# Optimization experiments

Measured on AMD Instinct MI355X. Metric: run time of the kernel, lower is better.

The kernel has to match this reference:

```python
import jax, jax.numpy as jnp
import numpy as np

DIM = 512
N_LAYERS = 2
N_HEADS = 8
HEAD_DIM = DIM // N_HEADS
VOCAB = 50257
MAX_SEQ = 2048
N_LEVELS = 3  # len(chunk_sizes)
HID = 4 * DIM
B, S = 2, 1024
STD = 0.02
EPS = 1e-5


def setup_inputs() -> dict:
    key = jax.random.key(0)
    ks = jax.random.split(key, 12)
    f32 = jnp.float32
    inp = {}
    inp["input_ids"] = jax.random.randint(ks[0], (B, S), 0, VOCAB)
    inp["tok_emb"] = jax.random.normal(ks[1], (VOCAB, DIM), f32) * STD  # tied with head
    inp["pos_emb"] = jax.random.normal(ks[2], (MAX_SEQ, DIM), f32) * STD
    # attention projections, stored [in, out] so y = x @ W (math-equivalent to torch x @ W.T)
    inp["Wq"] = jax.random.normal(ks[3], (N_LAYERS, DIM, DIM), f32) * STD
    inp["Wk"] = jax.random.normal(ks[4], (N_LAYERS, DIM, DIM), f32) * STD
    inp["Wv"] = jax.random.normal(ks[5], (N_LAYERS, DIM, DIM), f32) * STD
    inp["Wo"] = jax.random.normal(ks[6], (N_LAYERS, DIM, DIM), f32) * STD
    # layer norms
    inp["ln1_g"] = jnp.ones((N_LAYERS, DIM), f32)
    inp["ln1_b"] = jnp.zeros((N_LAYERS, DIM), f32)
    inp["ln2_g"] = jnp.ones((N_LAYERS, DIM), f32)
    inp["ln2_b"] = jnp.zeros((N_LAYERS, DIM), f32)
    inp["lnf_g"] = jnp.ones((DIM,), f32)
    inp["lnf_b"] = jnp.zeros((DIM,), f32)
    # continuum memory system: N_LEVELS chained MLPs per layer
    inp["W1"] = jax.random.normal(ks[7], (N_LAYERS, N_LEVELS, DIM, HID), f32) * STD
    inp["b1"] = jnp.zeros((N_LAYERS, N_LEVELS, HID), f32)
    inp["W2"] = jax.random.normal(ks[8], (N_LAYERS, N_LEVELS, HID, DIM), f32) * STD
    inp["b2"] = jnp.zeros((N_LAYERS, N_LEVELS, DIM), f32)
    return inp


def layer_norm(x, g, b):
    mu = jnp.mean(x, axis=-1, keepdims=True)
    var = jnp.var(x, axis=-1, keepdims=True)
    return (x - mu) / jnp.sqrt(var + EPS) * g + b


def linear_attention_with_memory(x, Wq, Wk, Wv, Wo):
    # x: [B, S, D]. Fast-weight recurrence: M_t = M_{t-1} + v_t k_t^T ; y_t = M_t q_t
    Bsz, Slen, D = x.shape
    H, hd = N_HEADS, HEAD_DIM

    def proj(W):  # -> [S, B, H, hd] (time-major for scan)
        return jnp.moveaxis((x @ W).reshape(Bsz, Slen, H, hd), 1, 0)

    q, k, v = proj(Wq), proj(Wk), proj(Wv)
    M0 = jnp.zeros((Bsz, H, hd, hd), x.dtype)

    def step(M, qkv):
        q_t, k_t, v_t = qkv
        M = M + jnp.einsum('bhd,bhk->bhdk', v_t, k_t)
        y_t = jnp.einsum('bhdk,bhk->bhd', M, q_t)
        return M, y_t

    _, ys = jax.lax.scan(step, M0, (q, k, v))  # ys: [S, B, H, hd]
    y = jnp.moveaxis(ys, 0, 1).reshape(Bsz, Slen, D)
    return y @ Wo


def cms(x, W1, b1, W2, b2):
    # chained MLP levels (dropout=0 / eval mode)
    for m in range(W1.shape[0]):
        x = jax.nn.gelu(x @ W1[m] + b1[m]) @ W2[m] + b2[m]
    return x


def reference(input_ids, tok_emb, pos_emb, Wq, Wk, Wv, Wo,
              ln1_g, ln1_b, ln2_g, ln2_b, lnf_g, lnf_b,
              W1, b1, W2, b2):
    Bsz, Slen = input_ids.shape
    x = tok_emb[input_ids] + pos_emb[:Slen][None, :, :]
    for l in range(Wq.shape[0]):
        x = x + linear_attention_with_memory(layer_norm(x, ln1_g[l], ln1_b[l]),
                                             Wq[l], Wk[l], Wv[l], Wo[l])
        x = x + cms(layer_norm(x, ln2_g[l], ln2_b[l]), W1[l], b1[l], W2[l], b2[l])
    x = layer_norm(x, lnf_g, lnf_b)
    logits = x @ tok_emb.T  # tied head
    return logits
```

## Files before the change

kernel.cpp:

```cpp
#include <hip/hip_runtime.h>
#include <hip/hip_bf16.h>
#include <cstdint>

using bf16 = __hip_bfloat16;
typedef __attribute__((ext_vector_type(8))) __bf16 bf16x8;
typedef __attribute__((ext_vector_type(4))) float f32x4;
typedef __attribute__((ext_vector_type(4))) unsigned int u32x4;

#define SEQ    1024
#define BATCH  2
#define ROWS   (BATCH*SEQ)
#define DMODEL 512
#define HIDDEN 2048
#define NHEADS 8
#define HD     64
#define VOCABN 50257
#define CHUNK  32
#define NCHUNK (SEQ/CHUNK)
#define QKVW   1536

__device__ __forceinline__ float gelu_tanh(float x) {
  float u = 0.7978845608028654f * (x + 0.044715f * x * x * x);
  return 0.5f * x * (1.0f + tanhf(u));
}

__global__ __launch_bounds__(512, 2)
void head_gemm8(const bf16* __restrict__ A, const bf16* __restrict__ Bt,
                float* __restrict__ C, int N, int ntn)
{
  constexpr int NT = 16;
  __shared__ __align__(16) bf16 Al[2 * 256 * 32];
  __shared__ __align__(16) bf16 Bl[2 * 256 * 32];
  const int t = threadIdx.x, lane = t & 63;
  const int w = t >> 6, wm = w >> 2, wn = w & 3;
  const int tm = blockIdx.x & 7, tn = blockIdx.x >> 3;
  const int arow0 = tm * 256, brow0 = tn * 256;
  const int rA = lane & 15;
  const int ko0 = lane >> 4;
  const int kph = ((ko0 ^ (rA & 3) ^ ((rA >> 2) & 3)) << 4);

  f32x4 acc[2][2][4][2];
#pragma unroll
  for (int i = 0; i < 2; ++i)
#pragma unroll
    for (int j = 0; j < 2; ++j)
#pragma unroll
      for (int m = 0; m < 4; ++m)
#pragma unroll
        for (int n = 0; n < 2; ++n) acc[i][j][m][n] = (f32x4){0.f, 0.f, 0.f, 0.f};

  auto stageA = [&](int s, int half, bf16* dstbuf) {
    int row = t >> 2, ko = t & 3;
    int kosrc = ko ^ (row & 3) ^ ((row >> 2) & 3);
    const bf16* src = A + (size_t)(arow0 + half * 128 + row) * 512 + s * 32 + kosrc * 8;
    bf16* dst = dstbuf + (half * 128 + row) * 32 + ko * 8;
    __builtin_amdgcn_global_load_lds(
        (const __attribute__((address_space(1))) unsigned int*)src,
        (__attribute__((address_space(3))) unsigned int*)dst, 16, 0, 0);
  };
  auto stageB = [&](int s, int half, bf16* dstbuf) {
    int row = t >> 2, ko = t & 3;
    int kosrc = ko ^ (row & 3) ^ ((row >> 2) & 3);
    int br = brow0 + half * 128 + row; br = br < N ? br : N - 1;
    const bf16* src = Bt + (size_t)br * 512 + s * 32 + kosrc * 8;
    bf16* dst = dstbuf + (half * 128 + row) * 32 + ko * 8;
    __builtin_amdgcn_global_load_lds(
        (const __attribute__((address_space(1))) unsigned int*)src,
        (__attribute__((address_space(3))) unsigned int*)dst, 16, 0, 0);
  };

  bf16* Ac = Al;
  bf16* Bc = Bl;
  bf16* An = Al + 8192;
  bf16* Bn = Bl + 8192;

  stageA(0, 0, Ac); stageB(0, 0, Bc); stageA(0, 1, Ac); stageB(0, 1, Bc);
  stageA(1, 0, An); stageB(1, 0, Bn);
  asm volatile("s_waitcnt vmcnt(2)" ::: "memory");
  asm volatile("s_barrier" ::: "memory");

#define PH(MH, NH, AC, BC, STAGE_STMT, WAIT_STMT) do {                          \
    bf16x8 a_[4], b_[2];                                                        \
    _Pragma("unroll") for (int fm = 0; fm < 4; ++fm) {                          \
      const char* ap = (const char*)(AC) +                                      \
          ((MH) * 128 + wm * 64 + fm * 16 + rA) * 64;                           \
      a_[fm] = __builtin_bit_cast(bf16x8, *(const u32x4*)(ap + kph));           \
    }                                                                           \
    _Pragma("unroll") for (int fn = 0; fn < 2; ++fn) {                          \
      const char* bp = (const char*)(BC) +                                      \
          ((NH) * 128 + wn * 32 + fn * 16 + rA) * 64;                           \
      b_[fn] = __builtin_bit_cast(bf16x8, *(const u32x4*)(bp + kph));           \
    }                                                                           \
    STAGE_STMT;                                                                 \
    asm volatile("s_barrier" ::: "memory");                                     \
    asm volatile("s_waitcnt lgkmcnt(0)" ::: "memory");                          \
    __builtin_amdgcn_sched_barrier(0);                                          \
    __builtin_amdgcn_s_setprio(1);                                              \
    _Pragma("unroll") for (int fm = 0; fm < 4; ++fm)                            \
      _Pragma("unroll") for (int fn = 0; fn < 2; ++fn)                          \
        acc[MH][NH][fm][fn] = __builtin_amdgcn_mfma_f32_16x16x32_bf16(          \
            a_[fm], b_[fn], acc[MH][NH][fm][fn], 0, 0, 0);                      \
    __builtin_amdgcn_s_setprio(0);                                              \
    WAIT_STMT;                                                                  \
    asm volatile("s_barrier" ::: "memory");                                     \
  } while (0)

#pragma unroll
  for (int I = 0; I < NT / 2; ++I) {
    const int u = 2 * I;
    PH(0, 0, Ac, Bc, { stageA(u + 1, 1, An); }, {});
    PH(0, 1, Ac, Bc, { stageB(u + 1, 1, Bn); }, {});
    PH(1, 0, Ac, Bc, { if (u + 2 < NT) stageA(u + 2, 0, Ac); }, {});
    PH(1, 1, Ac, Bc, { if (u + 2 < NT) stageB(u + 2, 0, Bc); },
       { if (u + 2 < NT) asm volatile("s_waitcnt vmcnt(2)" ::: "memory");
         else            asm volatile("s_waitcnt vmcnt(0)" ::: "memory"); });
    PH(0, 0, An, Bn, { if (u + 2 < NT) stageA(u + 2, 1, Ac); }, {});
    PH(0, 1, An, Bn, { if (u + 2 < NT) stageB(u + 2, 1, Bc); }, {});
    PH(1, 0, An, Bn, { if (u + 3 < NT) stageA(u + 3, 0, An); }, {});
    PH(1, 1, An, Bn, { if (u + 3 < NT) stageB(u + 3, 0, Bn); },
       { if (u + 2 < NT) {
           if (u + 3 < NT) asm volatile("s_waitcnt vmcnt(2)" ::: "memory");
           else            asm volatile("s_waitcnt vmcnt(0)" ::: "memory");
         } });
  }
#undef PH

#pragma unroll
  for (int mh = 0; mh < 2; ++mh)
#pragma unroll
    for (int fm = 0; fm < 4; ++fm) {
      int row = arow0 + mh * 128 + wm * 64 + fm * 16 + (lane >> 4) * 4;
#pragma unroll
      for (int nh = 0; nh < 2; ++nh)
#pragma unroll
        for (int fn = 0; fn < 2; ++fn) {
          int col = brow0 + nh * 128 + wn * 32 + fn * 16 + (lane & 15);
          if (col < N) {
#pragma unroll
            for (int r = 0; r < 4; ++r)
              C[(size_t)(row + r) * N + col] = acc[mh][nh][fm][fn][r];
          }
        }
    }
}

template<int EPI>
__global__ __launch_bounds__(256, 4)
void gemm_mid(const bf16* __restrict__ A, const bf16* __restrict__ Bt,
              void* __restrict__ Cout, const float* __restrict__ bias,
              int M, int N, int K, int Ks, int ldc, int ntn)
{
  __shared__ __align__(16) bf16 As[128 * 64];
  __shared__ __align__(16) bf16 Bs[64 * 64];
  const int t = threadIdx.x;
  const int lane = t & 63;
  const int w = t >> 6;
  const int wr = w >> 1, wc = w & 1;
  const int tm = blockIdx.x / ntn, tn = blockIdx.x % ntn;
  const int sk = blockIdx.y;
  const int kbeg = sk * Ks;
  const int rA = lane & 15;
  const int ko0 = lane >> 4;

  f32x4 acc[4][2];
#pragma unroll
  for (int m = 0; m < 4; ++m)
#pragma unroll
    for (int n = 0; n < 2; ++n) acc[m][n] = (f32x4){0.f, 0.f, 0.f, 0.f};

  for (int k0 = kbeg; k0 < kbeg + Ks; k0 += 64) {
#pragma unroll
    for (int rep = 0; rep < 4; ++rep) {
      int c = rep * 256 + t;
      int row = c >> 3, ko = c & 7;
      const bf16* ga = A + (size_t)(tm * 128 + row) * K + k0 + (ko ^ (row & 7)) * 8;
      __builtin_amdgcn_global_load_lds(
          (const __attribute__((address_space(1))) unsigned int*)ga,
          (__attribute__((address_space(3))) unsigned int*)(As + row * 64 + ko * 8),
          16, 0, 0);
    }
#pragma unroll
    for (int rep = 0; rep < 2; ++rep) {
      int c = rep * 256 + t;
      int row = c >> 3, ko = c & 7;
      const bf16* gb = Bt + (size_t)(tn * 64 + row) * K + k0 + (ko ^ (row & 7)) * 8;
      __builtin_amdgcn_global_load_lds(
          (const __attribute__((address_space(1))) unsigned int*)gb,
          (__attribute__((address_space(3))) unsigned int*)(Bs + row * 64 + ko * 8),
          16, 0, 0);
    }
    asm volatile("s_waitcnt vmcnt(0)" ::: "memory");
    __syncthreads();

    {
      bf16x8 af[4], bfv[2];
#pragma unroll
      for (int m = 0; m < 4; ++m) {
        int row = wr * 64 + m * 16 + rA;
        af[m] = __builtin_bit_cast(bf16x8,
            *(const u32x4*)((const char*)As + row * 128 + ((ko0 ^ (row & 7)) << 4)));
      }
#pragma unroll
      for (int n = 0; n < 2; ++n) {
        int row = wc * 32 + n * 16 + rA;
        bfv[n] = __builtin_bit_cast(bf16x8,
            *(const u32x4*)((const char*)Bs + row * 128 + ((ko0 ^ (row & 7)) << 4)));
      }
#pragma unroll
      for (int m = 0; m < 4; ++m)
#pragma unroll
        for (int n = 0; n < 2; ++n)
          acc[m][n] = __builtin_amdgcn_mfma_f32_16x16x32_bf16(af[m], bfv[n], acc[m][n], 0, 0, 0);
    }
    {
      bf16x8 af[4], bfv[2];
#pragma unroll
      for (int m = 0; m < 4; ++m) {
        int row = wr * 64 + m * 16 + rA;
        af[m] = __builtin_bit_cast(bf16x8,
            *(const u32x4*)((const char*)As + row * 128 + (((ko0 ^ (row & 7)) << 4) ^ 64)));
      }
#pragma unroll
      for (int n = 0; n < 2; ++n) {
        int row = wc * 32 + n * 16 + rA;
        bfv[n] = __builtin_bit_cast(bf16x8,
            *(const u32x4*)((const char*)Bs + row * 128 + (((ko0 ^ (row & 7)) << 4) ^ 64)));
      }
#pragma unroll
      for (int m = 0; m < 4; ++m)
#pragma unroll
        for (int n = 0; n < 2; ++n)
          acc[m][n] = __builtin_amdgcn_mfma_f32_16x16x32_bf16(af[m], bfv[n], acc[m][n], 0, 0, 0);
    }
    __syncthreads();
  }

#pragma unroll
  for (int m = 0; m < 4; ++m) {
    const int row = tm * 128 + wr * 64 + m * 16 + (lane >> 4) * 4;
#pragma unroll
    for (int n = 0; n < 2; ++n) {
      const int col = tn * 64 + wc * 32 + n * 16 + rA;
#pragma unroll
      for (int r = 0; r < 4; ++r) {
        float v = acc[m][n][r];
        if (EPI == 0) {
          ((float*)Cout)[(size_t)(row + r) * ldc + col] = v;
        } else if (EPI == 1) {
          ((float*)Cout)[(size_t)sk * M * N + (size_t)(row + r) * N + col] = v;
        } else {
          v += bias[col]; v = gelu_tanh(v);
          ((bf16*)Cout)[(size_t)(row + r) * ldc + col] = __float2bfloat16(v);
        }
      }
    }
  }
}

__global__ __launch_bounds__(256)
void reduce_bias_bf16(const float* __restrict__ part, bf16* __restrict__ out,
                      const float* __restrict__ bias)
{
  int i = blockIdx.x * 256 + threadIdx.x;
  const float4* p4 = (const float4*)part;
  const size_t str = (size_t)ROWS * DMODEL / 4;
  float4 v = p4[i];
  float4 v1 = p4[i + str], v2 = p4[i + 2 * str], v3 = p4[i + 3 * str];
  v.x += v1.x + v2.x + v3.x; v.y += v1.y + v2.y + v3.y;
  v.z += v1.z + v2.z + v3.z; v.w += v1.w + v2.w + v3.w;
  float4 bb = ((const float4*)bias)[i & (DMODEL / 4 - 1)];
  v.x += bb.x; v.y += bb.y; v.z += bb.z; v.w += bb.w;
  union { bf16 h[4]; uint2 u; } cv;
  cv.h[0] = __float2bfloat16(v.x); cv.h[1] = __float2bfloat16(v.y);
  cv.h[2] = __float2bfloat16(v.z); cv.h[3] = __float2bfloat16(v.w);
  ((uint2*)out)[i] = cv.u;
}

template<bool BIAS>
__global__ __launch_bounds__(256)
void reduce_resid_ln(const float* __restrict__ part, float* __restrict__ x,
                     const float* __restrict__ bias, const float* __restrict__ g,
                     const float* __restrict__ b, bf16* __restrict__ xn)
{
  int lane = threadIdx.x & 63;
  int row = blockIdx.x * 4 + (threadIdx.x >> 6);
  const float4* p4 = (const float4*)part;
  const size_t str = (size_t)ROWS * DMODEL / 4;
  size_t base = (size_t)row * (DMODEL / 4) + lane * 2;
  float4 a0 = p4[base], a1 = p4[base + 1];
#pragma unroll
  for (int s = 1; s < 4; ++s) {
    float4 q0 = p4[base + s * str], q1 = p4[base + 1 + s * str];
    a0.x += q0.x; a0.y += q0.y; a0.z += q0.z; a0.w += q0.w;
    a1.x += q1.x; a1.y += q1.y; a1.z += q1.z; a1.w += q1.w;
  }
  if (BIAS) {
    float4 b0 = ((const float4*)bias)[lane * 2];
    float4 b1 = ((const float4*)bias)[lane * 2 + 1];
    a0.x += b0.x; a0.y += b0.y; a0.z += b0.z; a0.w += b0.w;
    a1.x += b1.x; a1.y += b1.y; a1.z += b1.z; a1.w += b1.w;
  }
  float4* xr = (float4*)(x + (size_t)row * DMODEL);
  float4 x0 = xr[lane * 2], x1 = xr[lane * 2 + 1];
  x0.x += a0.x; x0.y += a0.y; x0.z += a0.z; x0.w += a0.w;
  x1.x += a1.x; x1.y += a1.y; x1.z += a1.z; x1.w += a1.w;
  xr[lane * 2] = x0; xr[lane * 2 + 1] = x1;
  float s  = x0.x + x0.y + x0.z + x0.w + x1.x + x1.y + x1.z + x1.w;
  float ss = x0.x*x0.x + x0.y*x0.y + x0.z*x0.z + x0.w*x0.w
           + x1.x*x1.x + x1.y*x1.y + x1.z*x1.z + x1.w*x1.w;
#pragma unroll
  for (int off = 32; off > 0; off >>= 1) { s += __shfl_xor(s, off); ss += __shfl_xor(ss, off); }
  float mu = s * (1.f / DMODEL);
  float inv = rsqrtf(ss * (1.f / DMODEL) - mu * mu + 1e-5f);
  int c0 = lane * 8;
  float vv[8] = {x0.x, x0.y, x0.z, x0.w, x1.x, x1.y, x1.z, x1.w};
#pragma unroll
  for (int j = 0; j < 8; ++j)
    xn[(size_t)row * DMODEL + c0 + j] = __float2bfloat16((vv[j] - mu) * inv * g[c0 + j] + b[c0 + j]);
}

__global__ __launch_bounds__(256)
void embed_ln(const int* __restrict__ ids, const float* __restrict__ te,
              const float* __restrict__ pe, const float* __restrict__ g,
              const float* __restrict__ b, float* __restrict__ x, bf16* __restrict__ xn)
{
  int lane = threadIdx.x & 63;
  int row = blockIdx.x * 4 + (threadIdx.x >> 6);
  int sq = row & (SEQ - 1);
  int id = ids[row];
  const float4* tr = (const float4*)(te + (size_t)id * DMODEL);
  const float4* pr = (const float4*)(pe + (size_t)sq * DMODEL);
  float4 x0 = tr[lane * 2], x1 = tr[lane * 2 + 1];
  float4 p0 = pr[lane * 2], p1 = pr[lane * 2 + 1];
  x0.x += p0.x; x0.y += p0.y; x0.z += p0.z; x0.w += p0.w;
  x1.x += p1.x; x1.y += p1.y; x1.z += p1.z; x1.w += p1.w;
  float4* xr = (float4*)(x + (size_t)row * DMODEL);
  xr[lane * 2] = x0; xr[lane * 2 + 1] = x1;
  float s  = x0.x + x0.y + x0.z + x0.w + x1.x + x1.y + x1.z + x1.w;
  float ss = x0.x*x0.x + x0.y*x0.y + x0.z*x0.z + x0.w*x0.w
           + x1.x*x1.x + x1.y*x1.y + x1.z*x1.z + x1.w*x1.w;
#pragma unroll
  for (int off = 32; off > 0; off >>= 1) { s += __shfl_xor(s, off); ss += __shfl_xor(ss, off); }
  float mu = s * (1.f / DMODEL);
  float inv = rsqrtf(ss * (1.f / DMODEL) - mu * mu + 1e-5f);
  int c0 = lane * 8;
  float vv[8] = {x0.x, x0.y, x0.z, x0.w, x1.x, x1.y, x1.z, x1.w};
#pragma unroll
  for (int j = 0; j < 8; ++j)
    xn[(size_t)row * DMODEL + c0 + j] = __float2bfloat16((vv[j] - mu) * inv * g[c0 + j] + b[c0 + j]);
}

__global__ __launch_bounds__(256)
void transpose_cvt(const float* __restrict__ in, bf16* __restrict__ out, int R, int C)
{
  __shared__ float tile[32][33];
  int mat = blockIdx.z;
  const float* src = in + (size_t)mat * R * C;
  bf16* dst = out + (size_t)mat * R * C;
  int c0 = blockIdx.x * 32, r0 = blockIdx.y * 32;
  int tx = threadIdx.x, ty = threadIdx.y;
#pragma unroll
  for (int i = ty; i < 32; i += 8)
    tile[i][tx] = src[(size_t)(r0 + i) * C + c0 + tx];
  __syncthreads();
#pragma unroll
  for (int i = ty; i < 32; i += 8)
    dst[(size_t)(c0 + i) * R + r0 + tx] = __float2bfloat16(tile[tx][i]);
}

__global__ __launch_bounds__(256)
void transpose_qkv(const float* __restrict__ Wq, const float* __restrict__ Wk,
                   const float* __restrict__ Wv, bf16* __restrict__ out)
{
  __shared__ float tile[32][33];
  int z = blockIdx.z;
  int l = z / 3, p = z % 3;
  const float* src = (p == 0 ? Wq : (p == 1 ? Wk : Wv)) + (size_t)l * DMODEL * DMODEL;
  bf16* dst = out + (size_t)l * QKVW * DMODEL + (size_t)p * DMODEL * DMODEL;
  int c0 = blockIdx.x * 32, r0 = blockIdx.y * 32;
  int tx = threadIdx.x, ty = threadIdx.y;
#pragma unroll
  for (int i = ty; i < 32; i += 8)
    tile[i][tx] = src[(size_t)(r0 + i) * DMODEL + c0 + tx];
  __syncthreads();
#pragma unroll
  for (int i = ty; i < 32; i += 8)
    dst[(size_t)(c0 + i) * DMODEL + r0 + tx] = __float2bfloat16(tile[tx][i]);
}

__global__ void cvt_bf16_k(const float* __restrict__ in, bf16* __restrict__ out, int n4)
{
  int i = blockIdx.x * 256 + threadIdx.x;
  if (i >= n4) return;
  float4 v = ((const float4*)in)[i];
  union { bf16 h[4]; uint2 u; } cv;
  cv.h[0] = __float2bfloat16(v.x); cv.h[1] = __float2bfloat16(v.y);
  cv.h[2] = __float2bfloat16(v.z); cv.h[3] = __float2bfloat16(v.w);
  ((uint2*)out)[i] = cv.u;
}

__global__ __launch_bounds__(256)
void scan_ktv(const float* __restrict__ qkv, float* __restrict__ ktv)
{
  int blk = blockIdx.x;
  int c = blk & (NCHUNK - 1), bh = blk >> 5;
  int b = bh >> 3, h = bh & 7;
  __shared__ float ks[CHUNK][64], vs[CHUNK][64];
  int t = threadIdx.x;
  size_t base = ((size_t)(b * SEQ + c * CHUNK)) * QKVW + h * HD;
#pragma unroll
  for (int i = 0; i < CHUNK * 64 / 256; ++i) {
    int idx = i * 256 + t;
    int s = idx >> 6, e = idx & 63;
    ks[s][e] = qkv[base + 512 + (size_t)s * QKVW + e];
    vs[s][e] = qkv[base + 1024 + (size_t)s * QKVW + e];
  }
  __syncthreads();
  int e = t >> 2, d0 = (t & 3) * 16;
  float acc[16];
#pragma unroll
  for (int j = 0; j < 16; ++j) acc[j] = 0.f;
  for (int s = 0; s < CHUNK; ++s) {
    float kv = ks[s][e];
#pragma unroll
    for (int j = 0; j < 16; ++j) acc[j] += kv * vs[s][d0 + j];
  }
  float* o = ktv + (size_t)blk * 4096 + e * 64 + d0;
#pragma unroll
  for (int j = 0; j < 16; ++j) o[j] = acc[j];
}

__global__ __launch_bounds__(256)
void scan_attn(const float* __restrict__ qkv, const float* __restrict__ ktv,
               bf16* __restrict__ y)
{
  int blk = blockIdx.x;
  int c = blk & (NCHUNK - 1), bh = blk >> 5;
  int b = bh >> 3, h = bh & 7;
  __shared__ float qs[CHUNK][65], ks[CHUNK][65], vs[CHUNK][65];
  __shared__ float Ss[CHUNK][CHUNK + 1];
  __shared__ float Ms[64][65];
  int t = threadIdx.x;
  size_t base = ((size_t)(b * SEQ + c * CHUNK)) * QKVW + h * HD;
#pragma unroll
  for (int i = 0; i < CHUNK * 64 / 256; ++i) {
    int idx = i * 256 + t;
    int s = idx >> 6, e = idx & 63;
    qs[s][e] = qkv[base + (size_t)s * QKVW + e];
    ks[s][e] = qkv[base + 512 + (size_t)s * QKVW + e];
    vs[s][e] = qkv[base + 1024 + (size_t)s * QKVW + e];
  }
  {
    int e = t >> 2, d0 = (t & 3) * 16;
    float mp[16];
#pragma unroll
    for (int j = 0; j < 16; ++j) mp[j] = 0.f;
    for (int cp = 0; cp < c; ++cp) {
      const float* p = ktv + ((size_t)bh * NCHUNK + cp) * 4096 + e * 64 + d0;
#pragma unroll
      for (int j = 0; j < 16; ++j) mp[j] += p[j];
    }
#pragma unroll
    for (int j = 0; j < 16; ++j) Ms[e][d0 + j] = mp[j];
  }
  __syncthreads();
  {
    int si = t >> 3, j0 = (t & 7) * 4;
    float sa[4] = {0.f, 0.f, 0.f, 0.f};
    for (int e = 0; e < 64; ++e) {
      float qv = qs[si][e];
#pragma unroll
      for (int j = 0; j < 4; ++j) sa[j] += qv * ks[j0 + j][e];
    }
#pragma unroll
    for (int j = 0; j < 4; ++j) Ss[si][j0 + j] = (j0 + j <= si) ? sa[j] : 0.f;
  }
  __syncthreads();
  {
    int si = t >> 3, d0 = (t & 7) * 8;
    float ya[8];
#pragma unroll
    for (int j = 0; j < 8; ++j) ya[j] = 0.f;
    for (int sp = 0; sp < CHUNK; ++sp) {
      float sv = Ss[si][sp];
#pragma unroll
      for (int j = 0; j < 8; ++j) ya[j] += sv * vs[sp][d0 + j];
    }
    for (int e = 0; e < 64; ++e) {
      float qv = qs[si][e];
#pragma unroll
      for (int j = 0; j < 8; ++j) ya[j] += qv * Ms[e][d0 + j];
    }
    bf16* o = y + ((size_t)(b * SEQ + c * CHUNK + si)) * DMODEL + h * HD + d0;
#pragma unroll
    for (int j = 0; j < 8; ++j) o[j] = __float2bfloat16(ya[j]);
  }
}

extern "C" void kernel_launch(void* const* d_in, const int* in_sizes, int n_in,
                              void* d_out, int out_size, void* d_ws, size_t ws_size,
                              hipStream_t stream)
{
  const int*   ids  = (const int*)  d_in[0];
  const float* tok  = (const float*)d_in[1];
  const float* pos  = (const float*)d_in[2];
  const float* Wq   = (const float*)d_in[3];
  const float* Wk   = (const float*)d_in[4];
  const float* Wv   = (const float*)d_in[5];
  const float* Wo   = (const float*)d_in[6];
  const float* ln1g = (const float*)d_in[7];
  const float* ln1b = (const float*)d_in[8];
  const float* ln2g = (const float*)d_in[9];
  const float* ln2b = (const float*)d_in[10];
  const float* lnfg = (const float*)d_in[11];
  const float* lnfb = (const float*)d_in[12];
  const float* W1   = (const float*)d_in[13];
  const float* b1   = (const float*)d_in[14];
  const float* W2   = (const float*)d_in[15];
  const float* b2   = (const float*)d_in[16];
  float* out = (float*)d_out;

  char* ws = (char*)d_ws;
  size_t off = 0;
  auto alloc = [&](size_t bytes) { void* p = ws + off; off += (bytes + 255) & ~(size_t)255; return p; };
  bf16* QKVt = (bf16*)alloc((size_t)2 * QKVW * 512 * 2);
  bf16* Wot  = (bf16*)alloc((size_t)2 * 512 * 512 * 2);
  bf16* W1t  = (bf16*)alloc((size_t)6 * 512 * 2048 * 2);
  bf16* W2t  = (bf16*)alloc((size_t)6 * 2048 * 512 * 2);
  bf16* tokb = (bf16*)alloc((size_t)VOCABN * 512 * 2);
  float* x   = (float*)alloc((size_t)ROWS * 512 * 4);
  bf16*  xn  = (bf16*) alloc((size_t)ROWS * 512 * 2);
  bf16*  tbuf= (bf16*) alloc((size_t)ROWS * 512 * 2);
  bf16*  hbuf= (bf16*) alloc((size_t)ROWS * 2048 * 2);
  float* qkvf= (float*)alloc((size_t)ROWS * QKVW * 4);
  bf16*  yb  = (bf16*) alloc((size_t)ROWS * 512 * 2);
  float* ktv = (float*)alloc((size_t)16 * NCHUNK * 4096 * 4);
  float* part= (float*)alloc((size_t)4 * ROWS * 512 * 4);

  dim3 tb(32, 8);
  transpose_qkv<<<dim3(16, 16, 6), tb, 0, stream>>>(Wq, Wk, Wv, QKVt);
  transpose_cvt<<<dim3(16, 16, 2), tb, 0, stream>>>(Wo, Wot, 512, 512);
  transpose_cvt<<<dim3(64, 16, 6), tb, 0, stream>>>(W1, W1t, 512, 2048);
  transpose_cvt<<<dim3(16, 64, 6), tb, 0, stream>>>(W2, W2t, 2048, 512);
  int n4 = VOCABN * 512 / 4;
  cvt_bf16_k<<<(n4 + 255) / 256, 256, 0, stream>>>(tok, tokb, n4);

  embed_ln<<<ROWS / 4, 256, 0, stream>>>(ids, tok, pos, ln1g, ln1b, x, xn);

  for (int l = 0; l < 2; ++l) {
    gemm_mid<0><<<dim3(16 * (QKVW / 64)), 256, 0, stream>>>(
        xn, QKVt + (size_t)l * QKVW * 512, qkvf, nullptr, ROWS, QKVW, 512, 512, QKVW, QKVW / 64);
    scan_ktv<<<16 * NCHUNK, 256, 0, stream>>>(qkvf, ktv);
    scan_attn<<<16 * NCHUNK, 256, 0, stream>>>(qkvf, ktv, yb);
    gemm_mid<1><<<dim3(16 * 8, 4), 256, 0, stream>>>(
        yb, Wot + (size_t)l * 512 * 512, part, nullptr, ROWS, 512, 512, 128, 512, 8);
    reduce_resid_ln<false><<<ROWS / 4, 256, 0, stream>>>(
        part, x, nullptr, ln2g + l * 512, ln2b + l * 512, xn);

    const bf16* cur = xn;
    for (int m = 0; m < 3; ++m) {
      int lm = l * 3 + m;
      gemm_mid<2><<<dim3(16 * (2048 / 64)), 256, 0, stream>>>(
          cur, W1t + (size_t)lm * 2048 * 512, hbuf, b1 + (size_t)lm * 2048,
          ROWS, 2048, 512, 512, 2048, 2048 / 64);
      gemm_mid<1><<<dim3(16 * 8, 4), 256, 0, stream>>>(
          hbuf, W2t + (size_t)lm * 512 * 2048, part, nullptr, ROWS, 512, 2048, 512, 512, 8);
      if (m < 2) {
        reduce_bias_bf16<<<ROWS * 512 / 4 / 256, 256, 0, stream>>>(part, tbuf, b2 + (size_t)lm * 512);
        cur = tbuf;
      } else {
        const float* g = (l == 0) ? (ln1g + 512) : lnfg;
        const float* b = (l == 0) ? (ln1b + 512) : lnfb;
        reduce_resid_ln<true><<<ROWS / 4, 256, 0, stream>>>(part, x, b2 + (size_t)lm * 512, g, b, xn);
      }
    }
  }

  int ntn_h = (VOCABN + 255) / 256;
  head_gemm8<<<dim3(8 * ntn_h), 512, 0, stream>>>(xn, tokb, out, VOCABN, ntn_h);
}
```

Before: 653.3 us.

## Replace pipelined 256x256 head GEMM with single-buffered 128x256 tile kernel

Result: faster. 603.8 us (-7.6%).

```diff
diff --git a/kernel.cpp b/kernel.cpp
--- a/kernel.cpp
+++ b/kernel.cpp
@@ -25,123 +25,105 @@
 }
 
 __global__ __launch_bounds__(512, 2)
-void head_gemm8(const bf16* __restrict__ A, const bf16* __restrict__ Bt,
-                float* __restrict__ C, int N, int ntn)
-{
-  constexpr int NT = 16;
-  __shared__ __align__(16) bf16 Al[2 * 256 * 32];
-  __shared__ __align__(16) bf16 Bl[2 * 256 * 32];
+void head_sb(const bf16* __restrict__ A, const bf16* __restrict__ Bt,
+             float* __restrict__ C, int N)
+{
+  __shared__ __align__(16) bf16 As[128 * 64];
+  __shared__ __align__(16) bf16 Bs[256 * 64];
   const int t = threadIdx.x, lane = t & 63;
   const int w = t >> 6, wm = w >> 2, wn = w & 3;
-  const int tm = blockIdx.x & 7, tn = blockIdx.x >> 3;
-  const int arow0 = tm * 256, brow0 = tn * 256;
+  const int tm = blockIdx.x & 15, tn = blockIdx.x >> 4;
+  const int arow0 = tm * 128, brow0 = tn * 256;
   const int rA = lane & 15;
   const int ko0 = lane >> 4;
-  const int kph = ((ko0 ^ (rA & 3) ^ ((rA >> 2) & 3)) << 4);
-
-  f32x4 acc[2][2][4][2];
-#pragma unroll
-  for (int i = 0; i < 2; ++i)
-#pragma unroll
-    for (int j = 0; j < 2; ++j)
-#pragma unroll
-      for (int m = 0; m < 4; ++m)
-#pragma unroll
-        for (int n = 0; n < 2; ++n) acc[i][j][m][n] = (f32x4){0.f, 0.f, 0.f, 0.f};
-
-  auto stageA = [&](int s, int half, bf16* dstbuf) {
-    int row = t >> 2, ko = t & 3;
-    int kosrc = ko ^ (row & 3) ^ ((row >> 2) & 3);
-    const bf16* src = A + (size_t)(arow0 + half * 128 + row) * 512 + s * 32 + kosrc * 8;
-    bf16* dst = dstbuf + (half * 128 + row) * 32 + ko * 8;
-    __builtin_amdgcn_global_load_lds(
-        (const __attribute__((address_space(1))) unsigned int*)src,
-        (__attribute__((address_space(3))) unsigned int*)dst, 16, 0, 0);
-  };
-  auto stageB = [&](int s, int half, bf16* dstbuf) {
-    int row = t >> 2, ko = t & 3;
-    int kosrc = ko ^ (row & 3) ^ ((row >> 2) & 3);
-    int br = brow0 + half * 128 + row; br = br < N ? br : N - 1;
-    const bf16* src = Bt + (size_t)br * 512 + s * 32 + kosrc * 8;
-    bf16* dst = dstbuf + (half * 128 + row) * 32 + ko * 8;
-    __builtin_amdgcn_global_load_lds(
-        (const __attribute__((address_space(1))) unsigned int*)src,
-        (__attribute__((address_space(3))) unsigned int*)dst, 16, 0, 0);
-  };
-
-  bf16* Ac = Al;
-  bf16* Bc = Bl;
-  bf16* An = Al + 8192;
-  bf16* Bn = Bl + 8192;
-
-  stageA(0, 0, Ac); stageB(0, 0, Bc); stageA(0, 1, Ac); stageB(0, 1, Bc);
-  stageA(1, 0, An); stageB(1, 0, Bn);
-  asm volatile("s_waitcnt vmcnt(2)" ::: "memory");
-  asm volatile("s_barrier" ::: "memory");
-
-#define PH(MH, NH, AC, BC, STAGE_STMT, WAIT_STMT) do {                          \
-    bf16x8 a_[4], b_[2];                                                        \
-    _Pragma("unroll") for (int fm = 0; fm < 4; ++fm) {                          \
-      const char* ap = (const char*)(AC) +                                      \
-          ((MH) * 128 + wm * 64 + fm * 16 + rA) * 64;                           \
-      a_[fm] = __builtin_bit_cast(bf16x8, *(const u32x4*)(ap + kph));           \
-    }                                                                           \
-    _Pragma("unroll") for (int fn = 0; fn < 2; ++fn) {                          \
-      const char* bp = (const char*)(BC) +                                      \
-          ((NH) * 128 + wn * 32 + fn * 16 + rA) * 64;                           \
-      b_[fn] = __builtin_bit_cast(bf16x8, *(const u32x4*)(bp + kph));           \
-    }                                                                           \
-    STAGE_STMT;                                                                 \
-    asm volatile("s_barrier" ::: "memory");                                     \
-    asm volatile("s_waitcnt lgkmcnt(0)" ::: "memory");                          \
-    __builtin_amdgcn_sched_barrier(0);                                          \
-    __builtin_amdgcn_s_setprio(1);                                              \
-    _Pragma("unroll") for (int fm = 0; fm < 4; ++fm)                            \
-      _Pragma("unroll") for (int fn = 0; fn < 2; ++fn)                          \
-        acc[MH][NH][fm][fn] = __builtin_amdgcn_mfma_f32_16x16x32_bf16(          \
-            a_[fm], b_[fn], acc[MH][NH][fm][fn], 0, 0, 0);                      \
-    __builtin_amdgcn_s_setprio(0);                                              \
-    WAIT_STMT;                                                                  \
-    asm volatile("s_barrier" ::: "memory");                                     \
-  } while (0)
-
-#pragma unroll
-  for (int I = 0; I < NT / 2; ++I) {
-    const int u = 2 * I;
-    PH(0, 0, Ac, Bc, { stageA(u + 1, 1, An); }, {});
-    PH(0, 1, Ac, Bc, { stageB(u + 1, 1, Bn); }, {});
-    PH(1, 0, Ac, Bc, { if (u + 2 < NT) stageA(u + 2, 0, Ac); }, {});
-    PH(1, 1, Ac, Bc, { if (u + 2 < NT) stageB(u + 2, 0, Bc); },
-       { if (u + 2 < NT) asm volatile("s_waitcnt vmcnt(2)" ::: "memory");
-         else            asm volatile("s_waitcnt vmcnt(0)" ::: "memory"); });
-    PH(0, 0, An, Bn, { if (u + 2 < NT) stageA(u + 2, 1, Ac); }, {});
-    PH(0, 1, An, Bn, { if (u + 2 < NT) stageB(u + 2, 1, Bc); }, {});
-    PH(1, 0, An, Bn, { if (u + 3 < NT) stageA(u + 3, 0, An); }, {});
-    PH(1, 1, An, Bn, { if (u + 3 < NT) stageB(u + 3, 0, Bn); },
-       { if (u + 2 < NT) {
-           if (u + 3 < NT) asm volatile("s_waitcnt vmcnt(2)" ::: "memory");
-           else            asm volatile("s_waitcnt vmcnt(0)" ::: "memory");
-         } });
-  }
-#undef PH
-
-#pragma unroll
-  for (int mh = 0; mh < 2; ++mh)
-#pragma unroll
-    for (int fm = 0; fm < 4; ++fm) {
-      int row = arow0 + mh * 128 + wm * 64 + fm * 16 + (lane >> 4) * 4;
-#pragma unroll
-      for (int nh = 0; nh < 2; ++nh)
-#pragma unroll
-        for (int fn = 0; fn < 2; ++fn) {
-          int col = brow0 + nh * 128 + wn * 32 + fn * 16 + (lane & 15);
-          if (col < N) {
-#pragma unroll
-            for (int r = 0; r < 4; ++r)
-              C[(size_t)(row + r) * N + col] = acc[mh][nh][fm][fn][r];
-          }
-        }
-    }
+
+  f32x4 acc[4][4];
+#pragma unroll
+  for (int m = 0; m < 4; ++m)
+#pragma unroll
+    for (int n = 0; n < 4; ++n) acc[m][n] = (f32x4){0.f, 0.f, 0.f, 0.f};
+
+  for (int k0 = 0; k0 < 512; k0 += 64) {
+#pragma unroll
+    for (int rep = 0; rep < 2; ++rep) {
+      int c = rep * 512 + t;
+      int row = c >> 3, ko = c & 7;
+      const bf16* ga = A + (size_t)(arow0 + row) * 512 + k0 + (ko ^ (row & 7)) * 8;
+      __builtin_amdgcn_global_load_lds(
+          (const __attribute__((address_space(1))) unsigned int*)ga,
+          (__attribute__((address_space(3))) unsigned int*)(As + row * 64 + ko * 8),
+          16, 0, 0);
+    }
+#pragma unroll
+    for (int rep = 0; rep < 4; ++rep) {
+      int c = rep * 512 + t;
+      int row = c >> 3, ko = c & 7;
+      int br = brow0 + row; br = br < N ? br : N - 1;
+      const bf16* gb = Bt + (size_t)br * 512 + k0 + (ko ^ (row & 7)) * 8;
+      __builtin_amdgcn_global_load_lds(
+          (const __attribute__((address_space(1))) unsigned int*)gb,
+          (__attribute__((address_space(3))) unsigned int*)(Bs + row * 64 + ko * 8),
+          16, 0, 0);
+    }
+    asm volatile("s_waitcnt vmcnt(0)" ::: "memory");
+    __syncthreads();
+
+    {
+      bf16x8 af[4], bfv[4];
+#pragma unroll
+      for (int fm = 0; fm < 4; ++fm) {
+        int row = wm * 64 + fm * 16 + rA;
+        af[fm] = __builtin_bit_cast(bf16x8,
+            *(const u32x4*)((const char*)As + row * 128 + ((ko0 ^ (row & 7)) << 4)));
+      }
+#pragma unroll
+      for (int fn = 0; fn < 4; ++fn) {
+        int row = wn * 64 + fn * 16 + rA;
+        bfv[fn] = __builtin_bit_cast(bf16x8,
+            *(const u32x4*)((const char*)Bs + row * 128 + ((ko0 ^ (row & 7)) << 4)));
+      }
+#pragma unroll
+      for (int fm = 0; fm < 4; ++fm)
+#pragma unroll
+        for (int fn = 0; fn < 4; ++fn)
+          acc[fm][fn] = __builtin_amdgcn_mfma_f32_16x16x32_bf16(af[fm], bfv[fn], acc[fm][fn], 0, 0, 0);
+    }
+    {
+      bf16x8 af[4], bfv[4];
+#pragma unroll
+      for (int fm = 0; fm < 4; ++fm) {
+        int row = wm * 64 + fm * 16 + rA;
+        af[fm] = __builtin_bit_cast(bf16x8,
+            *(const u32x4*)((const char*)As + row * 128 + (((ko0 ^ (row & 7)) << 4) ^ 64)));
+      }
+#pragma unroll
+      for (int fn = 0; fn < 4; ++fn) {
+        int row = wn * 64 + fn * 16 + rA;
+        bfv[fn] = __builtin_bit_cast(bf16x8,
+            *(const u32x4*)((const char*)Bs + row * 128 + (((ko0 ^ (row & 7)) << 4) ^ 64)));
+      }
+#pragma unroll
+      for (int fm = 0; fm < 4; ++fm)
+#pragma unroll
+        for (int fn = 0; fn < 4; ++fn)
+          acc[fm][fn] = __builtin_amdgcn_mfma_f32_16x16x32_bf16(af[fm], bfv[fn], acc[fm][fn], 0, 0, 0);
+    }
+    __syncthreads();
+  }
+
+#pragma unroll
+  for (int fm = 0; fm < 4; ++fm) {
+    const int row = arow0 + wm * 64 + fm * 16 + (lane >> 4) * 4;
+#pragma unroll
+    for (int fn = 0; fn < 4; ++fn) {
+      const int col = brow0 + wn * 64 + fn * 16 + rA;
+      if (col < N) {
+#pragma unroll
+        for (int r = 0; r < 4; ++r)
+          C[(size_t)(row + r) * N + col] = acc[fm][fn][r];
+      }
+    }
+  }
 }
 
 template<int EPI>
@@ -577,5 +559,5 @@
   }
 
   int ntn_h = (VOCABN + 255) / 256;
-  head_gemm8<<<dim3(8 * ntn_h), 512, 0, stream>>>(xn, tokb, out, VOCABN, ntn_h);
-}
+  head_sb<<<dim3(16 * ntn_h), 512, 0, stream>>>(xn, tokb, out, VOCABN);
+}
```
